# Kernel optimization log

Measured on AMD Instinct MI355X. Metric: run time of the kernel, lower is better.

The kernel has to match this reference:

```python
import jax, jax.numpy as jnp
import numpy as np

N_NODES = 50000
N_EDGES = 800000
NUM_IN, NUM_HID, NUM_OUT = 512, 256, 64
EPS = 1e-12


def agnn_conv(x, src, dst, beta, num_nodes):
    # PyG AGNNConv: score(j->i) = beta * cos(x_i, x_j); softmax over incoming
    # edges of each target node i; out_i = sum_j alpha_ij * x_j.
    norm = jnp.maximum(jnp.linalg.norm(x, axis=1, keepdims=True), EPS)
    xn = x / norm                                      # [N, H]
    scores = beta * jnp.sum(xn[dst] * xn[src], axis=1)  # [E]
    m = jax.ops.segment_max(scores, dst, num_segments=num_nodes)
    e = jnp.exp(scores - m[dst])
    s = jax.ops.segment_sum(e, dst, num_segments=num_nodes)
    alpha = e / s[dst]                                  # [E]
    return jax.ops.segment_sum(alpha[:, None] * x[src], dst, num_segments=num_nodes)


def setup_inputs() -> dict:
    key = jax.random.key(0)
    ks = jax.random.split(key, 7)
    x = jax.random.normal(ks[0], (N_NODES, NUM_IN), dtype=jnp.float32)
    edge_index = jax.random.randint(ks[1], (2, N_EDGES), 0, N_NODES, dtype=jnp.int64)
    w1 = jax.random.normal(ks[2], (NUM_HID, NUM_IN), dtype=jnp.float32) / np.sqrt(NUM_IN)
    b1 = jnp.zeros((NUM_HID,), dtype=jnp.float32)
    beta2 = jnp.ones((1,), dtype=jnp.float32)
    w2 = jax.random.normal(ks[3], (NUM_OUT, NUM_HID), dtype=jnp.float32) / np.sqrt(NUM_HID)
    b2 = jnp.zeros((NUM_OUT,), dtype=jnp.float32)
    return {"x": x, "edge_index": edge_index, "w1": w1, "b1": b1,
            "beta2": beta2, "w2": w2, "b2": b2}


def reference(x, edge_index, w1, b1, beta2, w2, b2):
    n = x.shape[0]
    # add self-loops (PyG AGNNConv default add_self_loops=True)
    loops = jnp.arange(n, dtype=edge_index.dtype)
    src = jnp.concatenate([edge_index[0], loops])
    dst = jnp.concatenate([edge_index[1], loops])

    h = jax.nn.relu(x @ w1.T + b1)                       # [N, H] (eval: dropout = id)
    h = agnn_conv(h, src, dst, jnp.float32(1.0), n)      # prop1, fixed beta=1
    z1 = h
    h = agnn_conv(h, src, dst, beta2[0], n)              # prop2, learnable beta
    z2 = h
    logits = h @ w2.T + b2                               # [N, C]
    return (z1, z2, jax.nn.log_softmax(logits, axis=1))
```

## Files before the change

kernel.cpp:

```cpp
#include <hip/hip_runtime.h>

#define N_NODES 50000
#define N_EDGES 800000
#define ETOT (N_EDGES + N_NODES)
#define DIN 512
#define HID 256
#define NOUT 64
#define SCAN_CHUNK 2048

typedef __attribute__((ext_vector_type(8))) short short8;
typedef __attribute__((ext_vector_type(4))) float f32x4;
typedef __attribute__((ext_vector_type(4))) unsigned short us4;

__device__ __forceinline__ unsigned short f2bf(float f) {
  union { float f; unsigned u; } x; x.f = f;
  unsigned r = x.u + 0x7fff + ((x.u >> 16) & 1);
  return (unsigned short)(r >> 16);
}
__device__ __forceinline__ float bf2f(unsigned short b) {
  return __uint_as_float(((unsigned)b) << 16);
}

#define AS1(p) ((const __attribute__((address_space(1))) unsigned int*)(p))
#define AS3(p) ((__attribute__((address_space(3))) unsigned int*)(p))

__device__ __forceinline__ int edge_at(const void* ei, long long idx, int is32) {
  if (is32) return ((const int*)ei)[idx];
  return (int)((const long long*)ei)[idx];
}

__global__ void initK(const void* ei, int* cursor, int* flag) {
  int i = blockIdx.x * blockDim.x + threadIdx.x;
  if (i < N_NODES) cursor[i] = 1;
  if (blockIdx.x == 0 && threadIdx.x < 64) {
    int lane = threadIdx.x;
    bool bad = false;
#pragma unroll
    for (int j = 0; j < 32; ++j) {
      long long v = ((const long long*)ei)[lane * 32 + j];
      bad |= (v < 0 || v >= N_NODES);
    }
    bool anybad = __any(bad);
    if (lane == 0) *flag = anybad ? 1 : 0;
  }
}

__global__ void histK(const void* ei, const int* flag, int* cursor) {
  int e = blockIdx.x * blockDim.x + threadIdx.x;
  if (e >= N_EDGES) return;
  int f = *flag;
  int d = edge_at(ei, (long long)N_EDGES + e, f);
  atomicAdd(&cursor[d], 1);
}

__global__ void scan1K(const int* counts, int* excl, int* bsums) {
  __shared__ int sdata[256];
  int base = blockIdx.x * SCAN_CHUNK;
  int t = threadIdx.x;
  int local[8];
  int sum = 0;
#pragma unroll
  for (int j = 0; j < 8; ++j) {
    int idx = base + t * 8 + j;
    int v = (idx < N_NODES) ? counts[idx] : 0;
    local[j] = sum;
    sum += v;
  }
  sdata[t] = sum;
  __syncthreads();
  for (int off = 1; off < 256; off <<= 1) {
    int v = (t >= off) ? sdata[t - off] : 0;
    __syncthreads();
    sdata[t] += v;
    __syncthreads();
  }
  int texcl = (t == 0) ? 0 : sdata[t - 1];
#pragma unroll
  for (int j = 0; j < 8; ++j) {
    int idx = base + t * 8 + j;
    if (idx < N_NODES) excl[idx] = texcl + local[j];
  }
  if (t == 255) bsums[blockIdx.x] = sdata[255];
}

__global__ void scan2K(int* bsums, int nb) {
  if (threadIdx.x == 0 && blockIdx.x == 0) {
    int run = 0;
    for (int i = 0; i < nb; ++i) { int v = bsums[i]; bsums[i] = run; run += v; }
  }
}

__global__ void scan3K(int* row_ptr, const int* bsums, int* cursor) {
  int i = blockIdx.x * blockDim.x + threadIdx.x;
  if (i < N_NODES) {
    int v = row_ptr[i] + bsums[i >> 11];
    row_ptr[i] = v;
    cursor[i] = v;
    if (i == 0) row_ptr[N_NODES] = ETOT;
  }
}

__global__ void scatterK(const void* ei, const int* flag, int* cursor, int* col) {
  int e = blockIdx.x * blockDim.x + threadIdx.x;
  if (e < N_EDGES) {
    int f = *flag;
    int s = edge_at(ei, e, f);
    int d = edge_at(ei, (long long)N_EDGES + e, f);
    int pos = atomicAdd(&cursor[d], 1);
    col[pos] = s;
  } else if (e < N_EDGES + N_NODES) {
    int i = e - N_EDGES;
    int pos = atomicAdd(&cursor[i], 1);
    col[pos] = i;
  }
}

__global__ __launch_bounds__(256) void cvtK(const float* __restrict__ x,
                                            const float* __restrict__ w1,
                                            unsigned short* __restrict__ xb,
                                            unsigned short* __restrict__ wb) {
  const long long NX = (long long)N_NODES * DIN / 8;
  const long long NW = (long long)HID * DIN / 8;
  long long stride = (long long)gridDim.x * blockDim.x;
  for (long long c = (long long)blockIdx.x * blockDim.x + threadIdx.x;
       c < NX + NW; c += stride) {
    const float* src;
    unsigned short* dst;
    if (c < NX) { src = x + c * 8; dst = xb + c * 8; }
    else { src = w1 + (c - NX) * 8; dst = wb + (c - NX) * 8; }
    float4 v0 = ((const float4*)src)[0];
    float4 v1 = ((const float4*)src)[1];
    short8 s;
    s[0] = f2bf(v0.x); s[1] = f2bf(v0.y); s[2] = f2bf(v0.z); s[3] = f2bf(v0.w);
    s[4] = f2bf(v1.x); s[5] = f2bf(v1.y); s[6] = f2bf(v1.z); s[7] = f2bf(v1.w);
    *(short8*)dst = s;
  }
}

__global__ __launch_bounds__(256) void gemm1MF(const unsigned short* __restrict__ Ab,
                                               const unsigned short* __restrict__ Bb,
                                               const float* __restrict__ bias,
                                               unsigned short* __restrict__ C) {
  __shared__ short As[128 * 64];
  __shared__ short Bs[128 * 64];
  int t = threadIdx.x;
  int wv = t >> 6, ln = t & 63;
  int wr = wv >> 1, wc = wv & 1;
  int row0 = blockIdx.x * 128;
  int col0 = blockIdx.y * 128;

  int lr = ln >> 3, lc = ln & 7;
  int scol = ((lc ^ lr) << 3);

  int ar0 = row0 + lr;
  const unsigned short* bbase = &Bb[(long long)(col0 + lr) * DIN + scol];

  f32x4 acc[4][4];
#pragma unroll
  for (int mi = 0; mi < 4; ++mi)
#pragma unroll
    for (int ni = 0; ni < 4; ++ni) acc[mi][ni] = (f32x4){0.f, 0.f, 0.f, 0.f};

  int g = ln >> 4;
  int fr = ln & 15;

  for (int k0 = 0; k0 < DIN; k0 += 64) {
#pragma unroll
    for (int it = 0; it < 4; ++it) {
      int chunk = it * 4 + wv;
      int ar = ar0 + chunk * 8;
      if (ar >= N_NODES) ar = N_NODES - 1;
      const unsigned short* asrc = &Ab[(long long)ar * DIN + k0 + scol];
      __builtin_amdgcn_global_load_lds(AS1(asrc), AS3(&As[chunk * 512]), 16, 0, 0);
      const unsigned short* bsrc = bbase + k0 + (long long)chunk * 8 * DIN;
      __builtin_amdgcn_global_load_lds(AS1(bsrc), AS3(&Bs[chunk * 512]), 16, 0, 0);
    }
    __syncthreads();

#pragma unroll
    for (int kk = 0; kk < 2; ++kk) {
      short8 af[4], bfr[4];
#pragma unroll
      for (int mi = 0; mi < 4; ++mi) {
        int r = wr * 64 + mi * 16 + fr;
        int slot = (kk * 4 + g) ^ (r & 7);
        af[mi] = *(const short8*)&As[r * 64 + slot * 8];
      }
#pragma unroll
      for (int ni = 0; ni < 4; ++ni) {
        int c = wc * 64 + ni * 16 + fr;
        int slot = (kk * 4 + g) ^ (c & 7);
        bfr[ni] = *(const short8*)&Bs[c * 64 + slot * 8];
      }
#pragma unroll
      for (int mi = 0; mi < 4; ++mi)
#pragma unroll
        for (int ni = 0; ni < 4; ++ni)
          acc[mi][ni] = __builtin_amdgcn_mfma_f32_16x16x32_bf16(af[mi], bfr[ni], acc[mi][ni], 0, 0, 0);
    }
    __syncthreads();
  }

  int fq = ln >> 4;
#pragma unroll
  for (int ni = 0; ni < 4; ++ni) {
    int colv = col0 + wc * 64 + ni * 16 + fr;
    float bv = bias[colv];
#pragma unroll
    for (int mi = 0; mi < 4; ++mi) {
#pragma unroll
      for (int j = 0; j < 4; ++j) {
        int row = row0 + wr * 64 + mi * 16 + fq * 4 + j;
        if (row < N_NODES)
          C[(long long)row * HID + colv] = f2bf(fmaxf(acc[mi][ni][j] + bv, 0.f));
      }
    }
  }
}

__global__ __launch_bounds__(256) void normBF(const unsigned short* __restrict__ hb,
                                              float* __restrict__ invn) {
  int w = (blockIdx.x * 256 + threadIdx.x) >> 6;
  int lane = threadIdx.x & 63;
  if (w >= N_NODES) return;
  us4 v = *(const us4*)&hb[(long long)w * HID + lane * 4];
  float x = bf2f(v.x), y = bf2f(v.y), z = bf2f(v.z), ww = bf2f(v.w);
  float s = x * x + y * y + z * z + ww * ww;
#pragma unroll
  for (int off = 32; off >= 1; off >>= 1) s += __shfl_xor(s, off);
  if (lane == 0) invn[w] = 1.0f / fmaxf(sqrtf(s), 1e-12f);
}

__global__ __launch_bounds__(256) void convK(const unsigned short* __restrict__ hb,
                                             const float* __restrict__ invn,
                                             const int* __restrict__ row_ptr,
                                             const int* __restrict__ col,
                                             const float* __restrict__ beta_ptr,
                                             float* __restrict__ hout,
                                             unsigned short* __restrict__ hout_bf) {
  int w = (blockIdx.x * 256 + threadIdx.x) >> 6;
  int lane = threadIdx.x & 63;
  if (w >= N_NODES) return;
  int g = lane >> 4;
  int sub = lane & 15;
  float beta = beta_ptr ? beta_ptr[0] : 1.0f;
  float babs = fabsf(beta);

  const unsigned short* hrow = &hb[(long long)w * HID + sub * 16];
  short8 hia = *(const short8*)hrow;
  short8 hib = *(const short8*)(hrow + 8);
  float hi[16];
#pragma unroll
  for (int q = 0; q < 8; ++q) {
    hi[q] = bf2f((unsigned short)hia[q]);
    hi[8 + q] = bf2f((unsigned short)hib[q]);
  }
  float scale_i = invn[w] * beta;

  int e0 = row_ptr[w], e1 = row_ptr[w + 1];
  int nit = (e1 - e0 + 3) >> 2;
  float Z = 0.f;
  float acc[16];
#pragma unroll
  for (int q = 0; q < 16; ++q) acc[q] = 0.f;

  for (int it = 0; it < nit; ++it) {
    int ee = e0 + it * 4 + g;
    bool valid = ee < e1;
    int s = col[valid ? ee : (e1 - 1)];
    float is = invn[s];
    const unsigned short* hj = &hb[(long long)s * HID + sub * 16];
    short8 ja = *(const short8*)hj;
    short8 jb = *(const short8*)(hj + 8);
    float hjf[16];
#pragma unroll
    for (int q = 0; q < 8; ++q) {
      hjf[q] = bf2f((unsigned short)ja[q]);
      hjf[8 + q] = bf2f((unsigned short)jb[q]);
    }
    float p = 0.f;
#pragma unroll
    for (int q = 0; q < 16; ++q) p += hi[q] * hjf[q];
    p += __shfl_xor(p, 1);
    p += __shfl_xor(p, 2);
    p += __shfl_xor(p, 4);
    p += __shfl_xor(p, 8);
    float sc = p * scale_i * is;
    float wt = valid ? __expf(sc - babs) : 0.f;
    Z += wt;
#pragma unroll
    for (int q = 0; q < 16; ++q) acc[q] += wt * hjf[q];
  }

#pragma unroll
  for (int q = 0; q < 16; ++q) {
    acc[q] += __shfl_xor(acc[q], 16);
    acc[q] += __shfl_xor(acc[q], 32);
  }
  Z += __shfl_xor(Z, 16);
  Z += __shfl_xor(Z, 32);
  float r = 1.0f / Z;

  if (g == 0) {
    float* po = &hout[(long long)w * HID + sub * 16];
#pragma unroll
    for (int q4 = 0; q4 < 4; ++q4) {
      float4 o;
      o.x = acc[q4 * 4 + 0] * r;
      o.y = acc[q4 * 4 + 1] * r;
      o.z = acc[q4 * 4 + 2] * r;
      o.w = acc[q4 * 4 + 3] * r;
      *(float4*)&po[q4 * 4] = o;
    }
  } else if (g == 1 && hout_bf) {
    unsigned short* pb = &hout_bf[(long long)w * HID + sub * 16];
#pragma unroll
    for (int q4 = 0; q4 < 4; ++q4) {
      us4 ob;
      ob.x = f2bf(acc[q4 * 4 + 0] * r);
      ob.y = f2bf(acc[q4 * 4 + 1] * r);
      ob.z = f2bf(acc[q4 * 4 + 2] * r);
      ob.w = f2bf(acc[q4 * 4 + 3] * r);
      *(us4*)&pb[q4 * 4] = ob;
    }
  }
}

__global__ __launch_bounds__(256) void headK2(const float* __restrict__ Z,
                                              const float* __restrict__ W,
                                              const float* __restrict__ bias,
                                              float* __restrict__ out) {
  __shared__ float smem[2 * 32 * 68];
  float* As = smem;
  float* Bs = smem + 32 * 68;
  int t = threadIdx.x;
  int tx = t & 15, ty = t >> 4;
  int row0 = blockIdx.x * 64;
  float acc[4][4] = {};
  int lr = t >> 3;
  int lc4 = t & 7;

  for (int k0 = 0; k0 < HID; k0 += 32) {
#pragma unroll
    for (int rr = 0; rr < 64; rr += 32) {
      int gr = row0 + lr + rr;
      float4 va = (gr < N_NODES)
                      ? *(const float4*)&Z[(long long)gr * HID + k0 + lc4 * 4]
                      : make_float4(0.f, 0.f, 0.f, 0.f);
      As[(lc4 * 4 + 0) * 68 + lr + rr] = va.x;
      As[(lc4 * 4 + 1) * 68 + lr + rr] = va.y;
      As[(lc4 * 4 + 2) * 68 + lr + rr] = va.z;
      As[(lc4 * 4 + 3) * 68 + lr + rr] = va.w;
      int gc = lr + rr;
      float4 vb = *(const float4*)&W[(long long)gc * HID + k0 + lc4 * 4];
      Bs[(lc4 * 4 + 0) * 68 + lr + rr] = vb.x;
      Bs[(lc4 * 4 + 1) * 68 + lr + rr] = vb.y;
      Bs[(lc4 * 4 + 2) * 68 + lr + rr] = vb.z;
      Bs[(lc4 * 4 + 3) * 68 + lr + rr] = vb.w;
    }
    __syncthreads();
#pragma unroll
    for (int kk = 0; kk < 32; ++kk) {
      float4 a4 = *(const float4*)&As[kk * 68 + ty * 4];
      float4 b4 = *(const float4*)&Bs[kk * 68 + tx * 4];
      acc[0][0] += a4.x * b4.x; acc[0][1] += a4.x * b4.y; acc[0][2] += a4.x * b4.z; acc[0][3] += a4.x * b4.w;
      acc[1][0] += a4.y * b4.x; acc[1][1] += a4.y * b4.y; acc[1][2] += a4.y * b4.z; acc[1][3] += a4.y * b4.w;
      acc[2][0] += a4.z * b4.x; acc[2][1] += a4.z * b4.y; acc[2][2] += a4.z * b4.z; acc[2][3] += a4.z * b4.w;
      acc[3][0] += a4.w * b4.x; acc[3][1] += a4.w * b4.y; acc[3][2] += a4.w * b4.z; acc[3][3] += a4.w * b4.w;
    }
    __syncthreads();
  }

  float* ls = smem;
  float4 bv = *(const float4*)&bias[tx * 4];
#pragma unroll
  for (int r = 0; r < 4; ++r) {
    int lrow = ty * 4 + r;
    ls[lrow * 65 + tx * 4 + 0] = acc[r][0] + bv.x;
    ls[lrow * 65 + tx * 4 + 1] = acc[r][1] + bv.y;
    ls[lrow * 65 + tx * 4 + 2] = acc[r][2] + bv.z;
    ls[lrow * 65 + tx * 4 + 3] = acc[r][3] + bv.w;
  }
  __syncthreads();

  int wid = t >> 6, lane = t & 63;
#pragma unroll
  for (int rr2 = wid; rr2 < 64; rr2 += 4) {
    int node = row0 + rr2;
    if (node < N_NODES) {
      float v = ls[rr2 * 65 + lane];
      float mx = v;
#pragma unroll
      for (int off = 32; off >= 1; off >>= 1) mx = fmaxf(mx, __shfl_xor(mx, off));
      float ex = __expf(v - mx);
      float se = ex;
#pragma unroll
      for (int off = 32; off >= 1; off >>= 1) se += __shfl_xor(se, off);
      out[(long long)node * NOUT + lane] = v - mx - __logf(se);
    }
  }
}

extern "C" void kernel_launch(void* const* d_in, const int* in_sizes, int n_in,
                              void* d_out, int out_size, void* d_ws, size_t ws_size,
                              hipStream_t stream) {
  (void)in_sizes; (void)n_in; (void)out_size; (void)ws_size;
  const float* x = (const float*)d_in[0];
  const void* ei = d_in[1];
  const float* w1 = (const float*)d_in[2];
  const float* b1 = (const float*)d_in[3];
  const float* beta2 = (const float*)d_in[4];
  const float* w2 = (const float*)d_in[5];
  const float* b2 = (const float*)d_in[6];

  float* z1 = (float*)d_out;
  float* z2 = z1 + (size_t)N_NODES * HID;
  float* lsm = z2 + (size_t)N_NODES * HID;

  unsigned short* h_bf = (unsigned short*)d_ws;
  unsigned short* z1_bf = h_bf + (size_t)N_NODES * HID;
  float* invn = (float*)(z1_bf + (size_t)N_NODES * HID);
  int* row_ptr = (int*)(invn + N_NODES);
  int* cursor = row_ptr + N_NODES + 1;
  int* colv = cursor + N_NODES;
  int* bsums = colv + ETOT;
  int* flag = bsums + 64;
  unsigned short* wb = (unsigned short*)(flag + 4);

  unsigned short* xb = (unsigned short*)z2;

  int nScan = (N_NODES + SCAN_CHUNK - 1) / SCAN_CHUNK;

  cvtK<<<2048, 256, 0, stream>>>(x, w1, xb, wb);
  initK<<<(N_NODES + 255) / 256, 256, 0, stream>>>(ei, cursor, flag);

  dim3 gg((N_NODES + 127) / 128, HID / 128);
  gemm1MF<<<gg, 256, 0, stream>>>(xb, wb, b1, h_bf);

  histK<<<(N_EDGES + 255) / 256, 256, 0, stream>>>(ei, flag, cursor);
  scan1K<<<nScan, 256, 0, stream>>>(cursor, row_ptr, bsums);
  scan2K<<<1, 64, 0, stream>>>(bsums, nScan);
  scan3K<<<(N_NODES + 255) / 256, 256, 0, stream>>>(row_ptr, bsums, cursor);
  scatterK<<<(N_EDGES + N_NODES + 255) / 256, 256, 0, stream>>>(ei, flag, cursor, colv);

  normBF<<<(N_NODES + 3) / 4, 256, 0, stream>>>(h_bf, invn);
  convK<<<(N_NODES + 3) / 4, 256, 0, stream>>>(h_bf, invn, row_ptr, colv, nullptr, z1, z1_bf);
  normBF<<<(N_NODES + 3) / 4, 256, 0, stream>>>(z1_bf, invn);
  convK<<<(N_NODES + 3) / 4, 256, 0, stream>>>(z1_bf, invn, row_ptr, colv, beta2, z2, nullptr);

  headK2<<<(N_NODES + 63) / 64, 256, 0, stream>>>(z2, w2, b2, lsm);
}
```

Baseline: 364.0 us.

## Fuse fp32-to-bf16 conversion into GEMM and fold second norm into conv

Drops the standalone pass that converts x to bf16. The GEMM now loads fp32 x tiles straight into LDS and packs them to bf16 in registers with v_cvt_pk_bf16_f32, using a 64-row by full-256-column tile. The w1 conversion moves into initK, and the first conv kernel computes the inverse norms of its bf16 output, which removes the second normBF launch. The intent is to avoid writing and rereading the 51 MB bf16 copy of x. In exchange the GEMM moves twice the A bytes through LDS, works on a smaller K step with more syncs, and adds conversion ALU work inside the inner loop.

```diff
diff --git a/kernel.cpp b/kernel.cpp
--- a/kernel.cpp
+++ b/kernel.cpp
@@ -11,6 +11,7 @@
 typedef __attribute__((ext_vector_type(8))) short short8;
 typedef __attribute__((ext_vector_type(4))) float f32x4;
 typedef __attribute__((ext_vector_type(4))) unsigned short us4;
+typedef __attribute__((ext_vector_type(4))) unsigned int u32x4;
 
 __device__ __forceinline__ unsigned short f2bf(float f) {
   union { float f; unsigned u; } x; x.f = f;
@@ -20,6 +21,11 @@
 __device__ __forceinline__ float bf2f(unsigned short b) {
   return __uint_as_float(((unsigned)b) << 16);
 }
+__device__ __forceinline__ unsigned cvtpk(float a, float b) {
+  unsigned r;
+  asm("v_cvt_pk_bf16_f32 %0, %1, %2" : "=v"(r) : "v"(a), "v"(b));
+  return r;
+}
 
 #define AS1(p) ((const __attribute__((address_space(1))) unsigned int*)(p))
 #define AS3(p) ((__attribute__((address_space(3))) unsigned int*)(p))
@@ -29,9 +35,19 @@
   return (int)((const long long*)ei)[idx];
 }
 
-__global__ void initK(const void* ei, int* cursor, int* flag) {
+__global__ void initK(const void* ei, int* cursor, int* flag,
+                      const float* __restrict__ w1, unsigned short* __restrict__ wb) {
   int i = blockIdx.x * blockDim.x + threadIdx.x;
   if (i < N_NODES) cursor[i] = 1;
+  if (i < (HID * DIN) / 8) {
+    const float* src = w1 + i * 8;
+    float4 v0 = ((const float4*)src)[0];
+    float4 v1 = ((const float4*)src)[1];
+    short8 s;
+    s[0] = f2bf(v0.x); s[1] = f2bf(v0.y); s[2] = f2bf(v0.z); s[3] = f2bf(v0.w);
+    s[4] = f2bf(v1.x); s[5] = f2bf(v1.y); s[6] = f2bf(v1.z); s[7] = f2bf(v1.w);
+    *(short8*)(wb + i * 8) = s;
+  }
   if (blockIdx.x == 0 && threadIdx.x < 64) {
     int lane = threadIdx.x;
     bool bad = false;
@@ -115,45 +131,36 @@
   }
 }
 
-__global__ __launch_bounds__(256) void cvtK(const float* __restrict__ x,
-                                            const float* __restrict__ w1,
-                                            unsigned short* __restrict__ xb,
-                                            unsigned short* __restrict__ wb) {
-  const long long NX = (long long)N_NODES * DIN / 8;
-  const long long NW = (long long)HID * DIN / 8;
-  long long stride = (long long)gridDim.x * blockDim.x;
-  for (long long c = (long long)blockIdx.x * blockDim.x + threadIdx.x;
-       c < NX + NW; c += stride) {
-    const float* src;
-    unsigned short* dst;
-    if (c < NX) { src = x + c * 8; dst = xb + c * 8; }
-    else { src = w1 + (c - NX) * 8; dst = wb + (c - NX) * 8; }
-    float4 v0 = ((const float4*)src)[0];
-    float4 v1 = ((const float4*)src)[1];
-    short8 s;
-    s[0] = f2bf(v0.x); s[1] = f2bf(v0.y); s[2] = f2bf(v0.z); s[3] = f2bf(v0.w);
-    s[4] = f2bf(v1.x); s[5] = f2bf(v1.y); s[6] = f2bf(v1.z); s[7] = f2bf(v1.w);
-    *(short8*)dst = s;
-  }
-}
-
-__global__ __launch_bounds__(256) void gemm1MF(const unsigned short* __restrict__ Ab,
+__global__ __launch_bounds__(256) void gemm1MF(const float* __restrict__ A,
                                                const unsigned short* __restrict__ Bb,
                                                const float* __restrict__ bias,
                                                unsigned short* __restrict__ C) {
-  __shared__ short As[128 * 64];
-  __shared__ short Bs[128 * 64];
+  __shared__ float As[64 * 32];
+  __shared__ short Bs[256 * 32];
   int t = threadIdx.x;
   int wv = t >> 6, ln = t & 63;
-  int wr = wv >> 1, wc = wv & 1;
-  int row0 = blockIdx.x * 128;
-  int col0 = blockIdx.y * 128;
-
-  int lr = ln >> 3, lc = ln & 7;
-  int scol = ((lc ^ lr) << 3);
-
-  int ar0 = row0 + lr;
-  const unsigned short* bbase = &Bb[(long long)(col0 + lr) * DIN + scol];
+  int wc = wv;
+  int row0 = blockIdx.x * 64;
+
+  int sA = ln & 7;
+  int rA[2], gA[2];
+  const float* srcA[2];
+#pragma unroll
+  for (int i = 0; i < 2; ++i) {
+    rA[i] = i * 32 + wv * 8 + (ln >> 3);
+    int gr = row0 + rA[i];
+    if (gr >= N_NODES) gr = N_NODES - 1;
+    gA[i] = gr;
+    srcA[i] = &A[(long long)gr * DIN + ((sA ^ (rA[i] & 7)) << 2)];
+  }
+  int sB = ln & 3;
+  const unsigned short* srcB[4];
+  int rB[4];
+#pragma unroll
+  for (int i = 0; i < 4; ++i) {
+    rB[i] = i * 64 + wv * 16 + (ln >> 2);
+    srcB[i] = &Bb[(long long)rB[i] * DIN + ((sB ^ (rB[i] & 3)) << 3)];
+  }
 
   f32x4 acc[4][4];
 #pragma unroll
@@ -164,53 +171,56 @@
   int g = ln >> 4;
   int fr = ln & 15;
 
-  for (int k0 = 0; k0 < DIN; k0 += 64) {
-#pragma unroll
-    for (int it = 0; it < 4; ++it) {
-      int chunk = it * 4 + wv;
-      int ar = ar0 + chunk * 8;
-      if (ar >= N_NODES) ar = N_NODES - 1;
-      const unsigned short* asrc = &Ab[(long long)ar * DIN + k0 + scol];
-      __builtin_amdgcn_global_load_lds(AS1(asrc), AS3(&As[chunk * 512]), 16, 0, 0);
-      const unsigned short* bsrc = bbase + k0 + (long long)chunk * 8 * DIN;
-      __builtin_amdgcn_global_load_lds(AS1(bsrc), AS3(&Bs[chunk * 512]), 16, 0, 0);
-    }
-    __syncthreads();
-
-#pragma unroll
-    for (int kk = 0; kk < 2; ++kk) {
-      short8 af[4], bfr[4];
-#pragma unroll
-      for (int mi = 0; mi < 4; ++mi) {
-        int r = wr * 64 + mi * 16 + fr;
-        int slot = (kk * 4 + g) ^ (r & 7);
-        af[mi] = *(const short8*)&As[r * 64 + slot * 8];
-      }
-#pragma unroll
-      for (int ni = 0; ni < 4; ++ni) {
-        int c = wc * 64 + ni * 16 + fr;
-        int slot = (kk * 4 + g) ^ (c & 7);
-        bfr[ni] = *(const short8*)&Bs[c * 64 + slot * 8];
-      }
-#pragma unroll
-      for (int mi = 0; mi < 4; ++mi)
-#pragma unroll
-        for (int ni = 0; ni < 4; ++ni)
-          acc[mi][ni] = __builtin_amdgcn_mfma_f32_16x16x32_bf16(af[mi], bfr[ni], acc[mi][ni], 0, 0, 0);
-    }
+  for (int k0 = 0; k0 < DIN; k0 += 32) {
+#pragma unroll
+    for (int i = 0; i < 2; ++i)
+      __builtin_amdgcn_global_load_lds(AS1(srcA[i] + k0),
+                                       AS3(&As[i * 1024 + wv * 256]), 16, 0, 0);
+#pragma unroll
+    for (int i = 0; i < 4; ++i)
+      __builtin_amdgcn_global_load_lds(AS1(srcB[i] + k0),
+                                       AS3(&Bs[i * 2048 + wv * 512]), 16, 0, 0);
+    __syncthreads();
+
+    short8 af[4], bfr[4];
+#pragma unroll
+    for (int mi = 0; mi < 4; ++mi) {
+      int r = mi * 16 + fr;
+      int s0 = (2 * g) ^ (r & 7);
+      int s1 = (2 * g + 1) ^ (r & 7);
+      f32x4 a0 = *(const f32x4*)&As[r * 32 + s0 * 4];
+      f32x4 a1 = *(const f32x4*)&As[r * 32 + s1 * 4];
+      u32x4 w;
+      w.x = cvtpk(a0[0], a0[1]);
+      w.y = cvtpk(a0[2], a0[3]);
+      w.z = cvtpk(a1[0], a1[1]);
+      w.w = cvtpk(a1[2], a1[3]);
+      af[mi] = __builtin_bit_cast(short8, w);
+    }
+#pragma unroll
+    for (int ni = 0; ni < 4; ++ni) {
+      int c = wc * 64 + ni * 16 + fr;
+      int slot = g ^ (c & 3);
+      bfr[ni] = *(const short8*)&Bs[c * 32 + slot * 8];
+    }
+#pragma unroll
+    for (int mi = 0; mi < 4; ++mi)
+#pragma unroll
+      for (int ni = 0; ni < 4; ++ni)
+        acc[mi][ni] = __builtin_amdgcn_mfma_f32_16x16x32_bf16(af[mi], bfr[ni], acc[mi][ni], 0, 0, 0);
     __syncthreads();
   }
 
   int fq = ln >> 4;
 #pragma unroll
   for (int ni = 0; ni < 4; ++ni) {
-    int colv = col0 + wc * 64 + ni * 16 + fr;
+    int colv = wc * 64 + ni * 16 + fr;
     float bv = bias[colv];
 #pragma unroll
     for (int mi = 0; mi < 4; ++mi) {
 #pragma unroll
       for (int j = 0; j < 4; ++j) {
-        int row = row0 + wr * 64 + mi * 16 + fq * 4 + j;
+        int row = row0 + mi * 16 + fq * 4 + j;
         if (row < N_NODES)
           C[(long long)row * HID + colv] = f2bf(fmaxf(acc[mi][ni][j] + bv, 0.f));
       }
@@ -237,7 +247,8 @@
                                              const int* __restrict__ col,
                                              const float* __restrict__ beta_ptr,
                                              float* __restrict__ hout,
-                                             unsigned short* __restrict__ hout_bf) {
+                                             unsigned short* __restrict__ hout_bf,
+                                             float* __restrict__ invn_out) {
   int w = (blockIdx.x * 256 + threadIdx.x) >> 6;
   int lane = threadIdx.x & 63;
   if (w >= N_NODES) return;
@@ -323,6 +334,20 @@
       ob.w = f2bf(acc[q4 * 4 + 3] * r);
       *(us4*)&pb[q4 * 4] = ob;
     }
+  }
+
+  if (invn_out) {
+    float ss = 0.f;
+#pragma unroll
+    for (int q = 0; q < 16; ++q) {
+      float v = bf2f(f2bf(acc[q] * r));
+      ss = fmaf(v, v, ss);
+    }
+    ss += __shfl_xor(ss, 1);
+    ss += __shfl_xor(ss, 2);
+    ss += __shfl_xor(ss, 4);
+    ss += __shfl_xor(ss, 8);
+    if (lane == 0) invn_out[w] = 1.0f / fmaxf(sqrtf(ss), 1e-12f);
   }
 }
 
@@ -426,16 +451,13 @@
   int* bsums = colv + ETOT;
   int* flag = bsums + 64;
   unsigned short* wb = (unsigned short*)(flag + 4);
-
-  unsigned short* xb = (unsigned short*)z2;
+  float* invn2 = (float*)(wb + (size_t)HID * DIN);
 
   int nScan = (N_NODES + SCAN_CHUNK - 1) / SCAN_CHUNK;
 
-  cvtK<<<2048, 256, 0, stream>>>(x, w1, xb, wb);
-  initK<<<(N_NODES + 255) / 256, 256, 0, stream>>>(ei, cursor, flag);
-
-  dim3 gg((N_NODES + 127) / 128, HID / 128);
-  gemm1MF<<<gg, 256, 0, stream>>>(xb, wb, b1, h_bf);
+  initK<<<(N_NODES + 255) / 256, 256, 0, stream>>>(ei, cursor, flag, w1, wb);
+
+  gemm1MF<<<(N_NODES + 63) / 64, 256, 0, stream>>>(x, wb, b1, h_bf);
 
   histK<<<(N_EDGES + 255) / 256, 256, 0, stream>>>(ei, flag, cursor);
   scan1K<<<nScan, 256, 0, stream>>>(cursor, row_ptr, bsums);
@@ -444,9 +466,8 @@
   scatterK<<<(N_EDGES + N_NODES + 255) / 256, 256, 0, stream>>>(ei, flag, cursor, colv);
 
   normBF<<<(N_NODES + 3) / 4, 256, 0, stream>>>(h_bf, invn);
-  convK<<<(N_NODES + 3) / 4, 256, 0, stream>>>(h_bf, invn, row_ptr, colv, nullptr, z1, z1_bf);
-  normBF<<<(N_NODES + 3) / 4, 256, 0, stream>>>(z1_bf, invn);
-  convK<<<(N_NODES + 3) / 4, 256, 0, stream>>>(z1_bf, invn, row_ptr, colv, beta2, z2, nullptr);
+  convK<<<(N_NODES + 3) / 4, 256, 0, stream>>>(h_bf, invn, row_ptr, colv, nullptr, z1, z1_bf, invn2);
+  convK<<<(N_NODES + 3) / 4, 256, 0, stream>>>(z1_bf, invn2, row_ptr, colv, beta2, z2, nullptr, nullptr);
 
   headK2<<<(N_NODES + 63) / 64, 256, 0, stream>>>(z2, w2, b2, lsm);
 }
```

Measured after the change: 361.5 us. No clear change (-0.7%).

## Fuse fp32-to-bf16 conversion of x into GEMM1 tile loads

Applied to the files above, without the earlier changes.

Removes the standalone conversion kernel that turned x (50000x512 fp32) into bf16. GEMM1 now streams fp32 tiles of x directly into LDS and packs them to bf16 with v_cvt_pk_bf16_f32 when loading MFMA fragments. The small w1 conversion moves into initK. This avoids one full read and write pass over x plus a launch, but doubles the A-tile LDS footprint (32KB fp32) and the global bytes per GEMM tile, which may lower occupancy.

```diff
diff --git a/kernel.cpp b/kernel.cpp
--- a/kernel.cpp
+++ b/kernel.cpp
@@ -11,6 +11,7 @@
 typedef __attribute__((ext_vector_type(8))) short short8;
 typedef __attribute__((ext_vector_type(4))) float f32x4;
 typedef __attribute__((ext_vector_type(4))) unsigned short us4;
+typedef __attribute__((ext_vector_type(4))) unsigned int u32x4;
 
 __device__ __forceinline__ unsigned short f2bf(float f) {
   union { float f; unsigned u; } x; x.f = f;
@@ -20,6 +21,11 @@
 __device__ __forceinline__ float bf2f(unsigned short b) {
   return __uint_as_float(((unsigned)b) << 16);
 }
+__device__ __forceinline__ unsigned cvtpk(float a, float b) {
+  unsigned r;
+  asm("v_cvt_pk_bf16_f32 %0, %1, %2" : "=v"(r) : "v"(a), "v"(b));
+  return r;
+}
 
 #define AS1(p) ((const __attribute__((address_space(1))) unsigned int*)(p))
 #define AS3(p) ((__attribute__((address_space(3))) unsigned int*)(p))
@@ -29,9 +35,19 @@
   return (int)((const long long*)ei)[idx];
 }
 
-__global__ void initK(const void* ei, int* cursor, int* flag) {
+__global__ void initK(const void* ei, int* cursor, int* flag,
+                      const float* __restrict__ w1, unsigned short* __restrict__ wb) {
   int i = blockIdx.x * blockDim.x + threadIdx.x;
   if (i < N_NODES) cursor[i] = 1;
+  if (i < (HID * DIN) / 8) {
+    const float* src = w1 + i * 8;
+    float4 v0 = ((const float4*)src)[0];
+    float4 v1 = ((const float4*)src)[1];
+    short8 s;
+    s[0] = f2bf(v0.x); s[1] = f2bf(v0.y); s[2] = f2bf(v0.z); s[3] = f2bf(v0.w);
+    s[4] = f2bf(v1.x); s[5] = f2bf(v1.y); s[6] = f2bf(v1.z); s[7] = f2bf(v1.w);
+    *(short8*)(wb + i * 8) = s;
+  }
   if (blockIdx.x == 0 && threadIdx.x < 64) {
     int lane = threadIdx.x;
     bool bad = false;
@@ -115,33 +131,11 @@
   }
 }
 
-__global__ __launch_bounds__(256) void cvtK(const float* __restrict__ x,
-                                            const float* __restrict__ w1,
-                                            unsigned short* __restrict__ xb,
-                                            unsigned short* __restrict__ wb) {
-  const long long NX = (long long)N_NODES * DIN / 8;
-  const long long NW = (long long)HID * DIN / 8;
-  long long stride = (long long)gridDim.x * blockDim.x;
-  for (long long c = (long long)blockIdx.x * blockDim.x + threadIdx.x;
-       c < NX + NW; c += stride) {
-    const float* src;
-    unsigned short* dst;
-    if (c < NX) { src = x + c * 8; dst = xb + c * 8; }
-    else { src = w1 + (c - NX) * 8; dst = wb + (c - NX) * 8; }
-    float4 v0 = ((const float4*)src)[0];
-    float4 v1 = ((const float4*)src)[1];
-    short8 s;
-    s[0] = f2bf(v0.x); s[1] = f2bf(v0.y); s[2] = f2bf(v0.z); s[3] = f2bf(v0.w);
-    s[4] = f2bf(v1.x); s[5] = f2bf(v1.y); s[6] = f2bf(v1.z); s[7] = f2bf(v1.w);
-    *(short8*)dst = s;
-  }
-}
-
-__global__ __launch_bounds__(256) void gemm1MF(const unsigned short* __restrict__ Ab,
+__global__ __launch_bounds__(256) void gemm1MF(const float* __restrict__ A,
                                                const unsigned short* __restrict__ Bb,
                                                const float* __restrict__ bias,
                                                unsigned short* __restrict__ C) {
-  __shared__ short As[128 * 64];
+  __shared__ float As[128 * 64];
   __shared__ short Bs[128 * 64];
   int t = threadIdx.x;
   int wv = t >> 6, ln = t & 63;
@@ -149,11 +143,22 @@
   int row0 = blockIdx.x * 128;
   int col0 = blockIdx.y * 128;
 
-  int lr = ln >> 3, lc = ln & 7;
-  int scol = ((lc ^ lr) << 3);
-
-  int ar0 = row0 + lr;
-  const unsigned short* bbase = &Bb[(long long)(col0 + lr) * DIN + scol];
+  const float* aptr[8];
+#pragma unroll
+  for (int i = 0; i < 8; ++i) {
+    int chunk = i * 4 + wv;
+    int r = chunk * 4 + (ln >> 4);
+    int gr = row0 + r;
+    if (gr >= N_NODES) gr = N_NODES - 1;
+    aptr[i] = &A[(long long)gr * DIN + (((ln & 15) ^ (r & 7)) << 2)];
+  }
+  const unsigned short* bptr[4];
+#pragma unroll
+  for (int i = 0; i < 4; ++i) {
+    int chunk = i * 4 + wv;
+    int r = chunk * 8 + (ln >> 3);
+    bptr[i] = &Bb[(long long)(col0 + r) * DIN + (((ln & 7) ^ (r & 7)) << 3)];
+  }
 
   f32x4 acc[4][4];
 #pragma unroll
@@ -166,15 +171,13 @@
 
   for (int k0 = 0; k0 < DIN; k0 += 64) {
 #pragma unroll
-    for (int it = 0; it < 4; ++it) {
-      int chunk = it * 4 + wv;
-      int ar = ar0 + chunk * 8;
-      if (ar >= N_NODES) ar = N_NODES - 1;
-      const unsigned short* asrc = &Ab[(long long)ar * DIN + k0 + scol];
-      __builtin_amdgcn_global_load_lds(AS1(asrc), AS3(&As[chunk * 512]), 16, 0, 0);
-      const unsigned short* bsrc = bbase + k0 + (long long)chunk * 8 * DIN;
-      __builtin_amdgcn_global_load_lds(AS1(bsrc), AS3(&Bs[chunk * 512]), 16, 0, 0);
-    }
+    for (int i = 0; i < 8; ++i)
+      __builtin_amdgcn_global_load_lds(AS1(aptr[i] + k0),
+                                       AS3(&As[(i * 4 + wv) * 256]), 16, 0, 0);
+#pragma unroll
+    for (int i = 0; i < 4; ++i)
+      __builtin_amdgcn_global_load_lds(AS1(bptr[i] + k0),
+                                       AS3(&Bs[(i * 4 + wv) * 512]), 16, 0, 0);
     __syncthreads();
 
 #pragma unroll
@@ -183,8 +186,16 @@
 #pragma unroll
       for (int mi = 0; mi < 4; ++mi) {
         int r = wr * 64 + mi * 16 + fr;
-        int slot = (kk * 4 + g) ^ (r & 7);
-        af[mi] = *(const short8*)&As[r * 64 + slot * 8];
+        int s0 = kk * 8 + ((2 * g) ^ (r & 7));
+        int s1 = kk * 8 + ((2 * g + 1) ^ (r & 7));
+        f32x4 a0 = *(const f32x4*)&As[r * 64 + s0 * 4];
+        f32x4 a1 = *(const f32x4*)&As[r * 64 + s1 * 4];
+        u32x4 pk;
+        pk.x = cvtpk(a0[0], a0[1]);
+        pk.y = cvtpk(a0[2], a0[3]);
+        pk.z = cvtpk(a1[0], a1[1]);
+        pk.w = cvtpk(a1[2], a1[3]);
+        af[mi] = __builtin_bit_cast(short8, pk);
       }
 #pragma unroll
       for (int ni = 0; ni < 4; ++ni) {
@@ -427,15 +438,12 @@
   int* flag = bsums + 64;
   unsigned short* wb = (unsigned short*)(flag + 4);
 
-  unsigned short* xb = (unsigned short*)z2;
-
   int nScan = (N_NODES + SCAN_CHUNK - 1) / SCAN_CHUNK;
 
-  cvtK<<<2048, 256, 0, stream>>>(x, w1, xb, wb);
-  initK<<<(N_NODES + 255) / 256, 256, 0, stream>>>(ei, cursor, flag);
+  initK<<<(N_NODES + 255) / 256, 256, 0, stream>>>(ei, cursor, flag, w1, wb);
 
   dim3 gg((N_NODES + 127) / 128, HID / 128);
-  gemm1MF<<<gg, 256, 0, stream>>>(xb, wb, b1, h_bf);
+  gemm1MF<<<gg, 256, 0, stream>>>(x, wb, b1, h_bf);
 
   histK<<<(N_EDGES + 255) / 256, 256, 0, stream>>>(ei, flag, cursor);
   scan1K<<<nScan, 256, 0, stream>>>(cursor, row_ptr, bsums);
```

After: 361.7 us. Within noise of the previous version (-0.6%).
